# Kernel tuning notes

Hardware: AMD Instinct MI355X
Metric: run time of the kernel (lower is better)

The kernel has to match this reference:

```python
import jax, jax.numpy as jnp
import numpy as np

EMBED = 1024
HEADS = 16
HEAD_DIM = EMBED // HEADS


def setup_inputs() -> dict:
    key = jax.random.key(0)
    ks = jax.random.split(key, 7)
    N, L = 2, 2048
    values = jax.random.normal(ks[0], (N, L, EMBED), dtype=jnp.float32)
    keys = jax.random.normal(ks[1], (N, L, EMBED), dtype=jnp.float32)
    queries = jax.random.normal(ks[2], (N, L, EMBED), dtype=jnp.float32)
    mask = jax.random.randint(ks[3], (N, 1, L, L), 0, 2, dtype=jnp.int32)
    s = 1.0 / np.sqrt(HEAD_DIM)
    Wv = jax.random.normal(ks[4], (HEAD_DIM, HEAD_DIM), dtype=jnp.float32) * s
    Wk = jax.random.normal(ks[5], (HEAD_DIM, HEAD_DIM), dtype=jnp.float32) * s
    Wq = jax.random.normal(ks[6], (HEAD_DIM, HEAD_DIM), dtype=jnp.float32) * s
    return {"values": values, "keys": keys, "queries": queries, "mask": mask,
            "Wv": Wv, "Wk": Wk, "Wq": Wq}


def reference(values, keys, queries, mask, Wv, Wk, Wq):
    N, Lq = queries.shape[0], queries.shape[1]
    Lk = keys.shape[1]
    # reshape to [N, L, H, D]; nn.Linear(x) = x @ W.T (shared across heads)
    v = values.reshape(N, Lk, HEADS, HEAD_DIM) @ Wv.T
    k = keys.reshape(N, Lk, HEADS, HEAD_DIM) @ Wk.T
    q = queries.reshape(N, Lq, HEADS, HEAD_DIM) @ Wq.T
    # scores scaled by sqrt(embed_size) as in the original module
    e = jnp.einsum("nqhd,nkhd->nhqk", q, k) / jnp.sqrt(jnp.float32(EMBED))
    e = jnp.where(mask == 0, jnp.float32(-1e20), e)
    attn = jax.nn.softmax(e, axis=-1)
    out = jnp.einsum("nhqk,nkhd->nqhd", attn, v)
    return out.reshape(N, Lq, HEADS * HEAD_DIM)
```

## Files before the change

kernel.cpp:

```cpp
#include <hip/hip_runtime.h>
#include <hip/hip_bf16.h>

#define LSEQ 2048
#define NB   2
#define NH   16
#define HD   64
#define NKT  32
#define QSCALE 0.04508687049285173f

typedef __attribute__((ext_vector_type(8)))  __bf16 bf16x8;
typedef __attribute__((ext_vector_type(4)))  __bf16 bf16x4;
typedef __attribute__((ext_vector_type(4)))  float  f32x4;
typedef __attribute__((ext_vector_type(16))) float  f32x16;
typedef __attribute__((ext_vector_type(2)))  unsigned long long u64x2;
typedef __attribute__((ext_vector_type(4)))  unsigned int u32x4;

__global__ __launch_bounds__(256)
void proj_kernel(const float* __restrict__ xv, const float* __restrict__ Wv_,
                 const float* __restrict__ xk, const float* __restrict__ Wk_,
                 const float* __restrict__ xq, const float* __restrict__ Wq_,
                 const int* __restrict__ mask,
                 __bf16* __restrict__ outv, __bf16* __restrict__ outk,
                 __bf16* __restrict__ outq,
                 unsigned long long* __restrict__ mbits) {
  __shared__ __bf16 S[16384];

  const int tid = threadIdx.x;

  if (blockIdx.z == 3) {
    const int bid  = blockIdx.x * NH + blockIdx.y;
    const int w    = tid >> 6;
    const int lane = tid & 63;
    const size_t wbase = (size_t)bid * 128 + w * 32;
#pragma unroll
    for (int i = 0; i < 8; ++i) {
      size_t g0 = wbase + i * 4;
#pragma unroll
      for (int j = 0; j < 4; ++j) {
        int v = mask[(g0 + j) * 64 + lane];
        unsigned long long b = __ballot(v != 0);
        if (lane == 0) mbits[g0 + j] = b;
      }
    }
    return;
  }

  __bf16* Xh = S;
  __bf16* Xl = S + 4096;
  __bf16* Wh = S + 8192;
  __bf16* Wl = S + 12288;

  const float* x; const float* W; __bf16* out;
  if (blockIdx.z == 0)      { x = xv; W = Wv_; out = outv; }
  else if (blockIdx.z == 1) { x = xk; W = Wk_; out = outk; }
  else                      { x = xq; W = Wq_; out = outq; }
  const float osc = (blockIdx.z == 2) ? QSCALE : 1.0f;

  const int bx = blockIdx.x;
  const int h  = blockIdx.y;
  const int n  = bx >> 5;
  const int l0 = (bx & 31) << 6;

  const int r  = tid >> 2;
  const int c0 = (tid & 3) << 4;
  const float* xrow = x + ((size_t)(n * LSEQ + l0) + r) * 1024 + h * 64 + c0;
  const float* wrow = W + r * 64 + c0;

#pragma unroll
  for (int hf = 0; hf < 2; ++hf) {
    int kc = c0 + hf * 8;
    int off = r * 64 + (kc ^ ((r & 7) << 3));
    float4 a = *(const float4*)(xrow + hf * 8);
    float4 b = *(const float4*)(xrow + hf * 8 + 4);
    float va[8] = {a.x, a.y, a.z, a.w, b.x, b.y, b.z, b.w};
    bf16x8 hi, lo;
#pragma unroll
    for (int j = 0; j < 8; ++j) {
      __bf16 h_ = (__bf16)va[j];
      hi[j] = h_;
      lo[j] = (__bf16)(va[j] - (float)h_);
    }
    *(bf16x8*)(Xh + off) = hi;
    *(bf16x8*)(Xl + off) = lo;

    float4 c = *(const float4*)(wrow + hf * 8);
    float4 d = *(const float4*)(wrow + hf * 8 + 4);
    float vw[8] = {c.x, c.y, c.z, c.w, d.x, d.y, d.z, d.w};
    bf16x8 whv, wlv;
#pragma unroll
    for (int j = 0; j < 8; ++j) {
      __bf16 h_ = (__bf16)vw[j];
      whv[j] = h_;
      wlv[j] = (__bf16)(vw[j] - (float)h_);
    }
    *(bf16x8*)(Wh + off) = whv;
    *(bf16x8*)(Wl + off) = wlv;
  }
  __syncthreads();

  const int wv   = tid >> 6;
  const int lane = tid & 63;
  const int l15  = lane & 15;
  const int lhi  = lane >> 4;

  bf16x8 xhf[2], xlf[2];
  const int arow = wv * 16 + l15;
#pragma unroll
  for (int ko = 0; ko < 2; ++ko) {
    int aoff = arow * 64 + ((ko * 32 + lhi * 8) ^ ((arow & 7) << 3));
    xhf[ko] = *(const bf16x8*)(Xh + aoff);
    xlf[ko] = *(const bf16x8*)(Xl + aoff);
  }

  f32x4 acc[4] = {};
#pragma unroll
  for (int cg = 0; cg < 4; ++cg) {
    int d = cg * 16 + l15;
#pragma unroll
    for (int ko = 0; ko < 2; ++ko) {
      int boff = d * 64 + ((ko * 32 + lhi * 8) ^ ((d & 7) << 3));
      bf16x8 whf = *(const bf16x8*)(Wh + boff);
      bf16x8 wlf = *(const bf16x8*)(Wl + boff);
      acc[cg] = __builtin_amdgcn_mfma_f32_16x16x32_bf16(xhf[ko], whf, acc[cg], 0, 0, 0);
      acc[cg] = __builtin_amdgcn_mfma_f32_16x16x32_bf16(xhf[ko], wlf, acc[cg], 0, 0, 0);
      acc[cg] = __builtin_amdgcn_mfma_f32_16x16x32_bf16(xlf[ko], whf, acc[cg], 0, 0, 0);
    }
  }
  __syncthreads();

  __bf16* tb = S;
#pragma unroll
  for (int cg = 0; cg < 4; ++cg)
#pragma unroll
    for (int rr = 0; rr < 4; ++rr)
      tb[(wv * 16 + lhi * 4 + rr) * 72 + cg * 16 + l15] = (__bf16)(acc[cg][rr] * osc);
  __syncthreads();

  if (blockIdx.z == 0) {
    const int d   = tid >> 2;
    const int cg  = tid & 3;
    const int swz = (d & 7) ^ ((d >> 3) & 7);
    __bf16* vout = out + (size_t)(n * NH + h) * (LSEQ * HD)
                 + (size_t)(bx & 31) * 4096 + d * 64 + cg * 16;
    bf16x8 s0, s1;
#pragma unroll
    for (int j16 = 0; j16 < 16; ++j16) {
      int c = cg * 16 + j16;
      int u = (c >> 3) ^ swz;
      int j = c & 7;
      int key = ((u >> 2) << 5) | (j & 3) | ((u & 1) << 2)
              | (((u >> 1) & 1) << 3) | ((j >> 2) << 4);
      __bf16 v_ = tb[key * 72 + d];
      if (j16 < 8) s0[j16] = v_; else s1[j16 - 8] = v_;
    }
    *(bf16x8*)(vout)     = s0;
    *(bf16x8*)(vout + 8) = s1;
  } else {
    const int tok = tid >> 2;
    const int d0  = (tid & 3) * 16;
    bf16x8 o0 = *(const bf16x8*)(tb + tok * 72 + d0);
    bf16x8 o1 = *(const bf16x8*)(tb + tok * 72 + d0 + 8);
    size_t ob = (size_t)(n * NH + h) * LSEQ + l0;
    *(bf16x8*)(out + (ob + tok) * HD + d0)     = o0;
    *(bf16x8*)(out + (ob + tok) * HD + d0 + 8) = o1;
  }
}

__global__ __launch_bounds__(512, 4)
void attn_kernel(const __bf16* __restrict__ Qb, const __bf16* __restrict__ Kb,
                 const __bf16* __restrict__ Vtp,
                 const unsigned long long* __restrict__ mbits,
                 float* __restrict__ out) {
  __shared__ __bf16 KV[32768];

  const int tid  = threadIdx.x;
  const int wid  = tid >> 6;
  const int hw   = wid >> 2;
  const int wq   = wid & 3;
  const int lane = tid & 63;
  const int l31  = lane & 31;
  const int hi5  = lane >> 5;

  const int lin = blockIdx.y * 16 + blockIdx.x;
  const int xcd = lin & 7;
  const int idx = lin >> 3;
  const int nh  = xcd + ((idx >> 4) << 3);
  const int qt  = idx & 15;
  const int n   = nh >> 4;
  const int h   = nh & 15;
  const int q0  = qt << 7;

  const __bf16* Qg = Qb + ((size_t)nh * LSEQ + q0) * HD;
  const __bf16* Kg = Kb + (size_t)nh * LSEQ * HD;
  const __bf16* Vg = Vtp + (size_t)nh * LSEQ * HD;

  const int qrow = wq * 32 + l31;
  bf16x8 qf[4];
#pragma unroll
  for (int ks = 0; ks < 4; ++ks)
    qf[ks] = *(const bf16x8*)(Qg + (size_t)qrow * HD + ks * 16 + hi5 * 8);

  f32x16 o0 = {}, o1 = {}, ols = {};
  const unsigned long long* mrow =
      mbits + ((size_t)n * LSEQ + q0 + qrow) * NKT;

  bf16x8 onesf;
#pragma unroll
  for (int j = 0; j < 8; ++j) onesf[j] = (__bf16)1.0f;

  const int key = hw * 32 + l31;
  const __bf16* kp[4];
#pragma unroll
  for (int ks = 0; ks < 4; ++ks)
    kp[ks] = &KV[key * 64 + (((2 * ks + hi5) ^ (key & 7)) << 3)];
  const __bf16* vp[4];
#pragma unroll
  for (int dh = 0; dh < 2; ++dh) {
    int d = dh * 32 + l31;
    int swz = (d & 7) ^ ((d >> 3) & 7);
    vp[dh * 2 + 0] = &KV[16384 + d * 64 + (((hw * 4 + hi5) ^ swz) << 3)];
    vp[dh * 2 + 1] = &KV[16384 + d * 64 + (((hw * 4 + 2 + hi5) ^ swz) << 3)];
  }

#define STAGE_K(kt_, buf_)                                                         \
  _Pragma("unroll")                                                                \
  for (int it = 0; it < 2; ++it) {                                                 \
    int chb = wq * 64 + it * 256;                                                  \
    int ch = chb + lane;                                                           \
    int skey = ch >> 3, sdc = ch & 7;                                              \
    const __bf16* src = Kg + (size_t)(kt_) * 4096 + skey * 64 + ((sdc ^ (skey & 7)) << 3); \
    __builtin_amdgcn_global_load_lds(                                              \
        (const __attribute__((address_space(1))) void*)src,                        \
        (__attribute__((address_space(3))) void*)(KV + (buf_) * 4096 + chb * 8), 16, 0, 0); \
  }
#define STAGE_V(kt_, buf_)                                                         \
  _Pragma("unroll")                                                                \
  for (int it = 0; it < 2; ++it) {                                                 \
    int chb = wq * 64 + it * 256;                                                  \
    int ch = chb + lane;                                                           \
    const __bf16* src = Vg + (size_t)(kt_) * 4096 + ch * 8;                        \
    __builtin_amdgcn_global_load_lds(                                              \
        (const __attribute__((address_space(1))) void*)src,                        \
        (__attribute__((address_space(3))) void*)(KV + 16384 + (buf_) * 4096 + chb * 8), 16, 0, 0); \
  }

#define PAIRW(s_, sh_, ra_, rb_, dstw_)                                            \
  {                                                                                \
    float pa_ = __builtin_amdgcn_exp2f(s_[ra_]);                                   \
    float pb_ = __builtin_amdgcn_exp2f(s_[rb_]);                                   \
    int ma_ = ((int)((sh_) << (31 - (((ra_) & 3) + 8 * ((ra_) >> 2))))) >> 31;     \
    int mb_ = ((int)((sh_) << (31 - (((rb_) & 3) + 8 * ((rb_) >> 2))))) >> 31;     \
    unsigned ua_ = __float_as_uint(pa_) & (unsigned)ma_;                           \
    unsigned ub_ = __float_as_uint(pb_) & (unsigned)mb_;                           \
    union { __hip_bfloat162 h2; unsigned u; } cv_;                                 \
    cv_.h2 = __float22bfloat162_rn(make_float2(__uint_as_float(ua_),               \
                                               __uint_as_float(ub_)));             \
    dstw_ = cv_.u;                                                                 \
  }

#define COMPUTE(W_, CB_)                                                           \
  {                                                                                \
    f32x16 s = {};                                                                 \
    _Pragma("unroll")                                                              \
    for (int ks = 0; ks < 4; ++ks) {                                               \
      bf16x8 kf = *(const bf16x8*)(kp[ks] + (CB_) * 4096);                         \
      s = __builtin_amdgcn_mfma_f32_32x32x16_bf16(kf, qf[ks], s, 0, 0, 0);         \
    }                                                                              \
    unsigned half_ = hw ? (unsigned)((W_) >> 32) : (unsigned)(W_);                 \
    unsigned sh = half_ >> (hi5 * 4);                                              \
    u32x4 w0_, w1_;                                                                \
    PAIRW(s, sh, 0, 1,  w0_[0]); PAIRW(s, sh, 2, 3,  w0_[1]);                      \
    PAIRW(s, sh, 8, 9,  w0_[2]); PAIRW(s, sh, 10, 11, w0_[3]);                     \
    PAIRW(s, sh, 4, 5,  w1_[0]); PAIRW(s, sh, 6, 7,  w1_[1]);                      \
    PAIRW(s, sh, 12, 13, w1_[2]); PAIRW(s, sh, 14, 15, w1_[3]);                    \
    bf16x8 pa0 = *(bf16x8*)&w0_;                                                   \
    bf16x8 pa1 = *(bf16x8*)&w1_;                                                   \
    {                                                                              \
      bf16x8 vf0 = *(const bf16x8*)(vp[0] + (CB_) * 4096);                         \
      bf16x8 vf1 = *(const bf16x8*)(vp[1] + (CB_) * 4096);                         \
      o0 = __builtin_amdgcn_mfma_f32_32x32x16_bf16(pa0, vf0, o0, 0, 0, 0);         \
      o0 = __builtin_amdgcn_mfma_f32_32x32x16_bf16(pa1, vf1, o0, 0, 0, 0);         \
      bf16x8 vf2 = *(const bf16x8*)(vp[2] + (CB_) * 4096);                         \
      bf16x8 vf3 = *(const bf16x8*)(vp[3] + (CB_) * 4096);                         \
      o1 = __builtin_amdgcn_mfma_f32_32x32x16_bf16(pa0, vf2, o1, 0, 0, 0);         \
      o1 = __builtin_amdgcn_mfma_f32_32x32x16_bf16(pa1, vf3, o1, 0, 0, 0);         \
    }                                                                              \
    ols = __builtin_amdgcn_mfma_f32_32x32x16_bf16(pa0, onesf, ols, 0, 0, 0);       \
    ols = __builtin_amdgcn_mfma_f32_32x32x16_bf16(pa1, onesf, ols, 0, 0, 0);       \
  }

  if (hw == 1) { STAGE_K(0, 0); STAGE_K(1, 1); }
  else         { STAGE_V(0, 0); STAGE_V(1, 1); }
  u64x2 wmA = *(const u64x2*)(mrow);
  u64x2 wmB = {0, 0};
  __syncthreads();

  for (int p8 = 0; p8 < 8; ++p8) {
    const int t0 = p8 * 4;
    if (hw == 1) { STAGE_K(t0 + 2, 2); STAGE_K(t0 + 3, 3); }
    else         { STAGE_V(t0 + 2, 2); STAGE_V(t0 + 3, 3); }
    wmB = *(const u64x2*)(mrow + t0 + 2);
    COMPUTE(wmA[0], 0);
    COMPUTE(wmA[1], 1);
    __syncthreads();
    if (p8 < 7) {
      if (hw == 1) { STAGE_K(t0 + 4, 0); STAGE_K(t0 + 5, 1); }
      else         { STAGE_V(t0 + 4, 0); STAGE_V(t0 + 5, 1); }
      wmA = *(const u64x2*)(mrow + t0 + 4);
    }
    COMPUTE(wmB[0], 2);
    COMPUTE(wmB[1], 3);
    __syncthreads();
  }

  float* Sf  = (float*)KV;
  float* Sl  = Sf + 8192;
  if (hw == 1) {
#pragma unroll
    for (int r = 0; r < 16; ++r) {
      Sf[((wq * 2 + 0) * 16 + r) * 64 + lane] = o0[r];
      Sf[((wq * 2 + 1) * 16 + r) * 64 + lane] = o1[r];
      Sl[(wq * 16 + r) * 64 + lane] = ols[r];
    }
  }
  __syncthreads();
  if (hw == 0) {
#pragma unroll
    for (int r = 0; r < 16; ++r) {
      float po0 = Sf[((wq * 2 + 0) * 16 + r) * 64 + lane];
      float po1 = Sf[((wq * 2 + 1) * 16 + r) * 64 + lane];
      float pls = Sl[(wq * 16 + r) * 64 + lane];
      float inv = 1.f / (ols[r] + pls);
      int qr = (r & 3) + 8 * (r >> 2) + 4 * hi5;
      size_t ob = ((size_t)n * LSEQ + q0 + wq * 32 + qr) * 1024 + h * 64 + l31;
      out[ob]      = (o0[r] + po0) * inv;
      out[ob + 32] = (o1[r] + po1) * inv;
    }
  }
#undef STAGE_K
#undef STAGE_V
#undef PAIRW
#undef COMPUTE
}

extern "C" void kernel_launch(void* const* d_in, const int* in_sizes, int n_in,
                              void* d_out, int out_size, void* d_ws, size_t ws_size,
                              hipStream_t stream) {
  const float* xv   = (const float*)d_in[0];
  const float* xk   = (const float*)d_in[1];
  const float* xq   = (const float*)d_in[2];
  const int*   mask = (const int*)d_in[3];
  const float* Wv   = (const float*)d_in[4];
  const float* Wk   = (const float*)d_in[5];
  const float* Wq   = (const float*)d_in[6];
  float* out = (float*)d_out;

  const size_t elems = (size_t)NB * NH * LSEQ * HD;
  __bf16* Qw = (__bf16*)d_ws;
  __bf16* Kw = Qw + elems;
  __bf16* Vw = Kw + elems;
  unsigned long long* mb = (unsigned long long*)(Vw + elems);

  proj_kernel<<<dim3(64, NH, 4), 256, 0, stream>>>(xv, Wv, xk, Wk, xq, Wq, mask,
                                                   Vw, Kw, Qw, mb);
  attn_kernel<<<dim3(16, 32), 512, 0, stream>>>(Qw, Kw, Vw, mb, out);
}
```

Before: 84.11 us.

## Halve attention block to 64 queries and double-buffer K/V staging

The attention kernel now uses 256-thread blocks covering 64 query rows instead of 512 threads covering 128, launching twice as many blocks, and its LDS footprint halves. The K/V staging moves from a four-buffer ring of two tiles per phase to a double buffer of one tile per sync. The aim is more resident blocks per CU and better load balance across the grid. In exchange, each K/V tile is reloaded by twice as many blocks, and the loop has twice as many barriers.

```diff
diff --git a/kernel.cpp b/kernel.cpp
--- a/kernel.cpp
+++ b/kernel.cpp
@@ -166,29 +166,29 @@
   }
 }
 
-__global__ __launch_bounds__(512, 4)
+__global__ __launch_bounds__(256, 4)
 void attn_kernel(const __bf16* __restrict__ Qb, const __bf16* __restrict__ Kb,
                  const __bf16* __restrict__ Vtp,
                  const unsigned long long* __restrict__ mbits,
                  float* __restrict__ out) {
-  __shared__ __bf16 KV[32768];
+  __shared__ __bf16 KV[16384];
 
   const int tid  = threadIdx.x;
   const int wid  = tid >> 6;
-  const int hw   = wid >> 2;
-  const int wq   = wid & 3;
+  const int hw   = wid >> 1;
+  const int wq   = wid & 1;
   const int lane = tid & 63;
   const int l31  = lane & 31;
   const int hi5  = lane >> 5;
 
-  const int lin = blockIdx.y * 16 + blockIdx.x;
+  const int lin = blockIdx.y * 32 + blockIdx.x;
   const int xcd = lin & 7;
   const int idx = lin >> 3;
-  const int nh  = xcd + ((idx >> 4) << 3);
-  const int qt  = idx & 15;
+  const int nh  = xcd + ((idx >> 5) << 3);
+  const int qt  = idx & 31;
   const int n   = nh >> 4;
   const int h   = nh & 15;
-  const int q0  = qt << 7;
+  const int q0  = qt << 6;
 
   const __bf16* Qg = Qb + ((size_t)nh * LSEQ + q0) * HD;
   const __bf16* Kg = Kb + (size_t)nh * LSEQ * HD;
@@ -218,14 +218,14 @@
   for (int dh = 0; dh < 2; ++dh) {
     int d = dh * 32 + l31;
     int swz = (d & 7) ^ ((d >> 3) & 7);
-    vp[dh * 2 + 0] = &KV[16384 + d * 64 + (((hw * 4 + hi5) ^ swz) << 3)];
-    vp[dh * 2 + 1] = &KV[16384 + d * 64 + (((hw * 4 + 2 + hi5) ^ swz) << 3)];
+    vp[dh * 2 + 0] = &KV[8192 + d * 64 + (((hw * 4 + hi5) ^ swz) << 3)];
+    vp[dh * 2 + 1] = &KV[8192 + d * 64 + (((hw * 4 + 2 + hi5) ^ swz) << 3)];
   }
 
 #define STAGE_K(kt_, buf_)                                                         \
   _Pragma("unroll")                                                                \
-  for (int it = 0; it < 2; ++it) {                                                 \
-    int chb = wq * 64 + it * 256;                                                  \
+  for (int it = 0; it < 4; ++it) {                                                 \
+    int chb = wq * 256 + it * 64;                                                  \
     int ch = chb + lane;                                                           \
     int skey = ch >> 3, sdc = ch & 7;                                              \
     const __bf16* src = Kg + (size_t)(kt_) * 4096 + skey * 64 + ((sdc ^ (skey & 7)) << 3); \
@@ -235,13 +235,13 @@
   }
 #define STAGE_V(kt_, buf_)                                                         \
   _Pragma("unroll")                                                                \
-  for (int it = 0; it < 2; ++it) {                                                 \
-    int chb = wq * 64 + it * 256;                                                  \
+  for (int it = 0; it < 4; ++it) {                                                 \
+    int chb = wq * 256 + it * 64;                                                  \
     int ch = chb + lane;                                                           \
     const __bf16* src = Vg + (size_t)(kt_) * 4096 + ch * 8;                        \
     __builtin_amdgcn_global_load_lds(                                              \
         (const __attribute__((address_space(1))) void*)src,                        \
-        (__attribute__((address_space(3))) void*)(KV + 16384 + (buf_) * 4096 + chb * 8), 16, 0, 0); \
+        (__attribute__((address_space(3))) void*)(KV + 8192 + (buf_) * 4096 + chb * 8), 16, 0, 0); \
   }
 
 #define PAIRW(s_, sh_, ra_, rb_, dstw_)                                            \
@@ -289,32 +289,29 @@
     ols = __builtin_amdgcn_mfma_f32_32x32x16_bf16(pa1, onesf, ols, 0, 0, 0);       \
   }
 
-  if (hw == 1) { STAGE_K(0, 0); STAGE_K(1, 1); }
-  else         { STAGE_V(0, 0); STAGE_V(1, 1); }
-  u64x2 wmA = *(const u64x2*)(mrow);
-  u64x2 wmB = {0, 0};
-  __syncthreads();
-
-  for (int p8 = 0; p8 < 8; ++p8) {
-    const int t0 = p8 * 4;
-    if (hw == 1) { STAGE_K(t0 + 2, 2); STAGE_K(t0 + 3, 3); }
-    else         { STAGE_V(t0 + 2, 2); STAGE_V(t0 + 3, 3); }
-    wmB = *(const u64x2*)(mrow + t0 + 2);
-    COMPUTE(wmA[0], 0);
-    COMPUTE(wmA[1], 1);
+  if (hw == 1) { STAGE_K(0, 0); }
+  else         { STAGE_V(0, 0); }
+  u64x2 wm = *(const u64x2*)(mrow);
+  __syncthreads();
+
+  for (int p = 0; p < 16; ++p) {
+    if (hw == 1) { STAGE_K(2 * p + 1, 1); }
+    else         { STAGE_V(2 * p + 1, 1); }
+    COMPUTE(wm[0], 0);
     __syncthreads();
-    if (p8 < 7) {
-      if (hw == 1) { STAGE_K(t0 + 4, 0); STAGE_K(t0 + 5, 1); }
-      else         { STAGE_V(t0 + 4, 0); STAGE_V(t0 + 5, 1); }
-      wmA = *(const u64x2*)(mrow + t0 + 4);
-    }
-    COMPUTE(wmB[0], 2);
-    COMPUTE(wmB[1], 3);
+    u64x2 nm = {0, 0};
+    if (p < 15) {
+      if (hw == 1) { STAGE_K(2 * p + 2, 0); }
+      else         { STAGE_V(2 * p + 2, 0); }
+      nm = *(const u64x2*)(mrow + 2 * p + 2);
+    }
+    COMPUTE(wm[1], 1);
+    wm = nm;
     __syncthreads();
   }
 
   float* Sf  = (float*)KV;
-  float* Sl  = Sf + 8192;
+  float* Sl  = Sf + 4096;
   if (hw == 1) {
 #pragma unroll
     for (int r = 0; r < 16; ++r) {
@@ -363,5 +360,5 @@
 
   proj_kernel<<<dim3(64, NH, 4), 256, 0, stream>>>(xv, Wv, xk, Wk, xq, Wq, mask,
                                                    Vw, Kw, Qw, mb);
-  attn_kernel<<<dim3(16, 32), 512, 0, stream>>>(Qw, Kw, Vw, mb, out);
+  attn_kernel<<<dim3(32, 32), 256, 0, stream>>>(Qw, Kw, Vw, mb, out);
 }
```

Result: slower. 99.75 us (+18.6%).
